# Kernel tuning notes

Hardware: AMD Instinct MI355X
Metric: run time of the kernel (lower is better)

## Reference

```python
import jax, jax.numpy as jnp
import numpy as np

B, N0, N1, FD, L, H = 4, 256, 256, 128, 3, 1
NG = N0 + N1            # nodes per graph
N = B * NG              # total nodes
EPS_BN = 1e-5
EPS_SM = 1e-16


def _build_edges():
    def perm_edges(n, off):
        idx = np.arange(n)
        a = np.repeat(idx, n); b = np.tile(idx, n)
        m = a != b
        return np.stack([a[m], b[m]]) + off
    e_intra = np.concatenate([perm_edges(N0, 0), perm_edges(N1, N0)], axis=1)
    a = np.arange(N0); b = np.arange(N0, N0 + N1)
    cross1 = np.stack([np.repeat(a, N1), np.tile(b, N0)])
    cross2 = np.stack([np.repeat(b, N0), np.tile(a, N1)])
    eg = np.concatenate([e_intra, cross1, cross2], axis=1)
    tg = np.concatenate([np.zeros(e_intra.shape[1], np.int32),
                         np.ones(cross1.shape[1] + cross2.shape[1], np.int32)])
    ei = np.concatenate([eg + g * NG for g in range(B)], axis=1).astype(np.int32)
    et = np.tile(tg, B).astype(np.int32)
    return jnp.asarray(ei), jnp.asarray(et)


def setup_inputs() -> dict:
    key = jax.random.key(0)
    ks = jax.random.split(key, 8)
    edge_index, edge_type = _build_edges()
    return {
        'desc0': jax.random.normal(ks[0], (B, FD, N0), jnp.float32),
        'desc1': jax.random.normal(ks[1], (B, FD, N1), jnp.float32),
        'W': jax.random.normal(ks[2], (L, 2, FD, H * FD), jnp.float32) * (1.0 / np.sqrt(FD)),
        'q': jax.random.normal(ks[3], (L, H * FD, H), jnp.float32) * 0.1,
        'k': jax.random.normal(ks[4], (L, H * FD, H), jnp.float32) * 0.1,
        'conv_b': jnp.zeros((L, FD), jnp.float32),
        'lin_W': jax.random.normal(ks[5], (L, FD, 2 * FD), jnp.float32) * (1.0 / np.sqrt(2 * FD)),
        'lin_b': jnp.zeros((L, FD), jnp.float32),
        'gamma': jnp.ones((L, FD), jnp.float32),
        'beta': jnp.zeros((L, FD), jnp.float32),
        'edge_index': edge_index,
        'edge_type': edge_type,
    }


def _forward(desc0, desc1, W, q, k, conv_b, lin_W, lin_b, gamma, beta, edge_index, edge_type):
    # x: [B, NG, FD] -> flattened batch graph [N, FD]
    x = jnp.concatenate([desc0, desc1], axis=2)        # [B, FD, NG]
    x = jnp.transpose(x, (0, 2, 1)).reshape(N, FD)
    src, dst = edge_index[0], edge_index[1]
    nlayers = W.shape[0]
    heads = q.shape[2]
    for l in range(nlayers):
        # relation-specific node projections (equiv to per-edge bmm with weight[edge_type])
        proj = jnp.einsum('nf,rfo->nro', x, W[l])       # [N, 2, H*FD]
        out_i = proj[dst, edge_type]                    # [E, H*FD]
        out_j = proj[src, edge_type]                    # [E, H*FD]
        alpha = jax.nn.leaky_relu(out_i @ q[l] + out_j @ k[l], 0.2)  # [E, H]
        # softmax over incoming edges of each destination node (across-relation)
        amax = jax.ops.segment_max(alpha, dst, num_segments=N)
        ex = jnp.exp(alpha - amax[dst])
        denom = jax.ops.segment_sum(ex, dst, num_segments=N)
        att = ex / (denom[dst] + EPS_SM)                # [E, H]
        msg = (att[:, :, None] * out_j.reshape(-1, heads, FD)).reshape(-1, heads * FD)
        agg = jax.ops.segment_sum(msg, dst, num_segments=N).reshape(N, heads, FD)
        m1 = jax.nn.relu(agg.mean(axis=1) + conv_b[l])  # concat=False -> mean over heads
        m2 = jnp.concatenate([x, m1], axis=1) @ lin_W[l].T + lin_b[l]
        mu = m2.mean(axis=0)
        var = ((m2 - mu) ** 2).mean(axis=0)             # biased var (BatchNorm training)
        m3 = (m2 - mu) / jnp.sqrt(var + EPS_BN) * gamma[l] + beta[l]
        x = x + m3
    x = x.reshape(B, NG, FD).transpose(0, 2, 1)         # [B, FD, NG]
    return x


def reference(desc0, desc1, W, q, k, conv_b, lin_W, lin_b, gamma, beta, edge_index, edge_type):
    x = _forward(desc0, desc1, W, q, k, conv_b, lin_W, lin_b, gamma, beta, edge_index, edge_type)
    return x[:, :, :N0], x[:, :, N0:]
```

## Files before the change

### kernel.cpp

```cpp
#include <hip/hip_runtime.h>

#define FD  128
#define NN  2048

#define OFF_X     0
#define OFF_PROJ  262144
#define OFF_QS    786432
#define OFF_KS    790528
#define OFF_SUMS  794624
#define OFF_LWT   800768
#define OFF_M2    899072

__device__ __forceinline__ int swizzle_n0(int bid) {
    int g    = (bid & 7) >> 1;
    int slot = ((bid >> 3) << 1) | (bid & 1);
    return g*512 + slot*8;
}

__device__ __forceinline__ void proj_qsks8(
    const float* __restrict__ W, const float* __restrict__ qv,
    const float* __restrict__ kv, float* __restrict__ ws,
    int l, int n0, int t, const float (*xs)[FD],
    float (*redp)[256], float* red)
{
    int kh = t >> 8, tp = t & 255;
    int rsel = tp >> 7, o = tp & 127;
    const float* Wl = W + ((size_t)(l*2 + rsel)*FD)*FD + o;
    float acc[8];
#pragma unroll
    for (int r = 0; r < 8; r++) acc[r] = 0.f;
    int kbase = kh * 64;
#pragma unroll
    for (int kk = 0; kk < 64; kk += 4) {
        int k4 = kbase + kk;
        float w0 = Wl[(k4+0)*FD], w1 = Wl[(k4+1)*FD];
        float w2 = Wl[(k4+2)*FD], w3 = Wl[(k4+3)*FD];
#pragma unroll
        for (int r = 0; r < 8; r++) {
            float4 xq = *(const float4*)&xs[r][k4];
            acc[r] += xq.x*w0 + xq.y*w1 + xq.z*w2 + xq.w*w3;
        }
    }
    if (kh == 1) {
#pragma unroll
        for (int r = 0; r < 8; r++) redp[r][tp] = acc[r];
    }
    __syncthreads();
    if (t < 256) {
#pragma unroll
        for (int r = 0; r < 8; r++) acc[r] += redp[r][tp];
#pragma unroll
        for (int r = 0; r < 8; r++)
            ws[OFF_PROJ + (size_t)(n0 + r)*256 + tp] = acc[r];

        float qq = qv[l*FD + o], kq = kv[l*FD + o];
        int lane = t & 63, w = t >> 6;
#pragma unroll
        for (int r = 0; r < 8; r++) {
            float vq = acc[r]*qq, vk = acc[r]*kq;
            for (int off = 32; off; off >>= 1) {
                vq += __shfl_xor(vq, off, 64);
                vk += __shfl_xor(vk, off, 64);
            }
            if (lane == 0) { red[w*16 + r*2] = vq; red[w*16 + r*2 + 1] = vk; }
        }
    }
    __syncthreads();
    if (t < 32) {
        int r = t & 7, rs = (t >> 3) & 1, wh = t >> 4;
        float v = red[(rs*2)*16 + r*2 + wh] + red[(rs*2 + 1)*16 + r*2 + wh];
        if (wh == 0) ws[OFF_QS + rs*NN + n0 + r] = v;
        else         ws[OFF_KS + rs*NN + n0 + r] = v;
    }
}

__global__ __launch_bounds__(512, 2) void k_pre(
    const float* __restrict__ d0, const float* __restrict__ d1,
    const float* __restrict__ W,  const float* __restrict__ qv,
    const float* __restrict__ kv, const float* __restrict__ linW,
    float* __restrict__ ws)
{
    int bid = blockIdx.x, t = threadIdx.x;
    if (bid >= 256) {
        if (bid < 280) {
            int vb = bid - 256;
#pragma unroll
            for (int i = 0; i < 8; i++) {
                int e = vb*4096 + i*512 + t;
                int l = e >> 15, rem = e & 32767;
                int o = rem >> 8, c = rem & 255;
                ws[OFF_LWT + l*32768 + c*FD + o] = linW[e];
            }
        } else {
            for (int i = t; i < 6144; i += 512) ws[OFF_SUMS + i] = 0.f;
        }
        return;
    }
    __shared__ __attribute__((aligned(16))) float xs[8][FD];
    __shared__ float redp[8][256];
    __shared__ float red[64];
    int n0 = swizzle_n0(bid);
#pragma unroll
    for (int i = 0; i < 2; i++) {
        int idx = t + i*512;
        int row = idx >> 7, f = idx & 127;
        int n = n0 + row, gg = n >> 9, ii = n & 511;
        float v = (ii < 256) ? d0[gg*32768 + f*256 + ii]
                             : d1[gg*32768 + f*256 + (ii - 256)];
        xs[row][f] = v;
        ws[OFF_X + (size_t)n*FD + f] = v;
    }
    __syncthreads();
    proj_qsks8(W, qv, kv, ws, 0, n0, t, xs, redp, red);
}

__global__ __launch_bounds__(512, 2) void k_bp(
    const float* __restrict__ W,     const float* __restrict__ qv,
    const float* __restrict__ kv,    const float* __restrict__ gamma,
    const float* __restrict__ beta,  float* __restrict__ ws, int l)
{
    __shared__ float scale[FD], shift[FD];
    __shared__ __attribute__((aligned(16))) float xs[8][FD];
    __shared__ float redp[8][256];
    __shared__ float red[64];
    int bid = blockIdx.x, t = threadIdx.x;
    int lp = l - 1;
    if (t < 128) {
        float s0 = 0.f, s1 = 0.f;
#pragma unroll
        for (int sl = 0; sl < 8; sl++) {
            s0 += ws[OFF_SUMS + lp*2048 + sl*256 + t];
            s1 += ws[OFF_SUMS + lp*2048 + sl*256 + 128 + t];
        }
        float mu  = s0 * (1.f/2048.f);
        float var = s1 * (1.f/2048.f) - mu*mu;
        float rs  = rsqrtf(var + 1e-5f);
        float gm  = gamma[lp*FD + t], bt = beta[lp*FD + t];
        scale[t] = gm * rs;
        shift[t] = bt - mu * gm * rs;
    }
    __syncthreads();
    int n0 = swizzle_n0(bid);
#pragma unroll
    for (int i = 0; i < 2; i++) {
        int idx = t + i*512;
        int row = idx >> 7, f = idx & 127;
        size_t e = (size_t)(n0 + row)*FD + f;
        float xv = ws[OFF_X + e] + ws[OFF_M2 + e]*scale[f] + shift[f];
        xs[row][f] = xv;
        ws[OFF_X + e] = xv;
    }
    __syncthreads();
    proj_qsks8(W, qv, kv, ws, l, n0, t, xs, redp, red);
}

__global__ __launch_bounds__(512, 2) void k_attn(
    const float* __restrict__ convb, const float* __restrict__ linb,
    float* __restrict__ ws, int l)
{
    __shared__ __attribute__((aligned(16))) float att[8*512];
    __shared__ __attribute__((aligned(16))) float redB[8*8*128];
    __shared__ __attribute__((aligned(16))) float cat[8*256];
    __shared__ float r1[FD], r2[FD];

    int bid = blockIdx.x, t = threadIdx.x;
    int dstbase = swizzle_n0(bid);
    int g = dstbase >> 9, dloc0 = dstbase & 511;
    int Gd = (dloc0 >= 256) ? 1 : 0;

    {
        int d = t >> 6, p = t & 63;
        int dloc = dloc0 + d;
        float q0 = ws[OFF_QS + dstbase + d];
        float q1 = ws[OFF_QS + NN + dstbase + d];
        float sc[8];
#pragma unroll
        for (int j = 0; j < 8; j++) {
            int s = p + j*64;
            int ts = (s < 256) ? Gd : 1 - Gd;
            float a = (ts ? q1 : q0) + ws[OFF_KS + ts*NN + g*512 + s];
            a = a > 0.f ? a : 0.2f*a;
            sc[j] = (s == dloc) ? -1e30f : a;
        }
        float lm = sc[0];
#pragma unroll
        for (int j = 1; j < 8; j++) lm = fmaxf(lm, sc[j]);
        for (int off = 32; off; off >>= 1) lm = fmaxf(lm, __shfl_xor(lm, off, 64));
        float ex[8], lsum = 0.f;
#pragma unroll
        for (int j = 0; j < 8; j++) { ex[j] = __expf(sc[j] - lm); lsum += ex[j]; }
        for (int off = 32; off; off >>= 1) lsum += __shfl_xor(lsum, off, 64);
        float inv = 1.f / (lsum + 1e-16f);
#pragma unroll
        for (int j = 0; j < 8; j++) att[d*512 + p + j*64] = ex[j]*inv;
        if (t < 128) r1[t] = 0.f;
        else if (t < 256) r2[t - 128] = 0.f;
    }
    __syncthreads();

    int f4 = t & 31, sq = t >> 5;
    float acc[8][4];
#pragma unroll
    for (int d2 = 0; d2 < 8; d2++)
#pragma unroll
        for (int j = 0; j < 4; j++) acc[d2][j] = 0.f;
    {
        int ts = (sq < 8) ? Gd : 1 - Gd;
        const float* P = ws + OFF_PROJ + (size_t)(g*512)*256 + ts*128 + f4*4;
        int s0 = sq * 32;
        float4 bufA[4], bufB[4];
#pragma unroll
        for (int u = 0; u < 4; u++) bufA[u] = *(const float4*)&P[(size_t)(s0+u)*256];
#pragma unroll
        for (int ii = 0; ii < 8; ii++) {
            const float4* cur = (ii & 1) ? bufB : bufA;
            float4*       nxt = (ii & 1) ? bufA : bufB;
            if (ii < 7) {
#pragma unroll
                for (int u = 0; u < 4; u++)
                    nxt[u] = *(const float4*)&P[(size_t)(s0 + (ii+1)*4 + u)*256];
            }
#pragma unroll
            for (int u = 0; u < 4; u++) {
                int s = s0 + ii*4 + u;
                float4 p4 = cur[u];
#pragma unroll
                for (int d2 = 0; d2 < 8; d2++) {
                    float b = att[d2*512 + s];
                    acc[d2][0] += b*p4.x; acc[d2][1] += b*p4.y;
                    acc[d2][2] += b*p4.z; acc[d2][3] += b*p4.w;
                }
            }
        }
    }
    if (sq >= 8) {
#pragma unroll
        for (int d2 = 0; d2 < 8; d2++)
            *(float4*)&redB[((sq - 8)*8 + d2)*128 + f4*4] =
                make_float4(acc[d2][0], acc[d2][1], acc[d2][2], acc[d2][3]);
    }
    __syncthreads();
    if (sq < 8) {
#pragma unroll
        for (int d2 = 0; d2 < 8; d2++) {
            float4 p4 = *(const float4*)&redB[(sq*8 + d2)*128 + f4*4];
            *(float4*)&redB[(sq*8 + d2)*128 + f4*4] =
                make_float4(acc[d2][0]+p4.x, acc[d2][1]+p4.y, acc[d2][2]+p4.z, acc[d2][3]+p4.w);
        }
    }
    __syncthreads();

    {
        int dh = t >> 7, f = t & 127;
#pragma unroll
        for (int half = 0; half < 2; half++) {
            int d2 = dh + half*4;
            float agg = 0.f;
#pragma unroll
            for (int cc = 0; cc < 8; cc++) agg += redB[(cc*8 + d2)*128 + f];
            float m1v = fmaxf(agg + convb[l*FD + f], 0.f);
            cat[d2*256 + FD + f] = m1v;
            cat[d2*256 + f] = ws[OFF_X + (size_t)(dstbase + d2)*FD + f];
        }
    }
    __syncthreads();

#pragma unroll
    for (int d2 = 0; d2 < 8; d2++)
#pragma unroll
        for (int j = 0; j < 4; j++) acc[d2][j] = 0.f;
    {
        const float* lwt = ws + OFF_LWT + l*32768 + f4*4;
        int c0 = sq * 16;
        float4 bufA[4], bufB[4];
#pragma unroll
        for (int u = 0; u < 4; u++) bufA[u] = *(const float4*)&lwt[(c0+u)*128];
#pragma unroll
        for (int ii = 0; ii < 4; ii++) {
            const float4* cur = (ii & 1) ? bufB : bufA;
            float4*       nxt = (ii & 1) ? bufA : bufB;
            if (ii < 3) {
#pragma unroll
                for (int u = 0; u < 4; u++)
                    nxt[u] = *(const float4*)&lwt[(c0 + (ii+1)*4 + u)*128];
            }
#pragma unroll
            for (int u = 0; u < 4; u++) {
                int c = c0 + ii*4 + u;
                float4 w4 = cur[u];
#pragma unroll
                for (int d2 = 0; d2 < 8; d2++) {
                    float cv = cat[d2*256 + c];
                    acc[d2][0] += cv*w4.x; acc[d2][1] += cv*w4.y;
                    acc[d2][2] += cv*w4.z; acc[d2][3] += cv*w4.w;
                }
            }
        }
    }
    if (sq >= 8) {
#pragma unroll
        for (int d2 = 0; d2 < 8; d2++)
            *(float4*)&redB[((sq - 8)*8 + d2)*128 + f4*4] =
                make_float4(acc[d2][0], acc[d2][1], acc[d2][2], acc[d2][3]);
    }
    __syncthreads();
    if (sq < 8) {
#pragma unroll
        for (int d2 = 0; d2 < 8; d2++) {
            float4 p4 = *(const float4*)&redB[(sq*8 + d2)*128 + f4*4];
            *(float4*)&redB[(sq*8 + d2)*128 + f4*4] =
                make_float4(acc[d2][0]+p4.x, acc[d2][1]+p4.y, acc[d2][2]+p4.z, acc[d2][3]+p4.w);
        }
    }
    __syncthreads();

    {
        int dh = t >> 7, o = t & 127;
        float lb = linb[l*FD + o];
#pragma unroll
        for (int half = 0; half < 2; half++) {
            int d2 = dh + half*4;
            float m2v = lb;
#pragma unroll
            for (int cc = 0; cc < 8; cc++) m2v += redB[(cc*8 + d2)*128 + o];
            ws[OFF_M2 + (size_t)(dstbase + d2)*FD + o] = m2v;
            atomicAdd(&r1[o], m2v);
            atomicAdd(&r2[o], m2v*m2v);
        }
    }
    __syncthreads();
    if (t < 128) {
        int slot = bid & 7;
        atomicAdd(&ws[OFF_SUMS + l*2048 + slot*256 + t],       r1[t]);
        atomicAdd(&ws[OFF_SUMS + l*2048 + slot*256 + 128 + t], r2[t]);
    }
}

__global__ __launch_bounds__(256) void k_bnout(
    const float* __restrict__ gamma, const float* __restrict__ beta,
    float* __restrict__ ws, float* __restrict__ out)
{
    __shared__ float scale[FD], shift[FD];
    int bid = blockIdx.x, t = threadIdx.x;
    if (t < 128) {
        float s0 = 0.f, s1 = 0.f;
#pragma unroll
        for (int sl = 0; sl < 8; sl++) {
            s0 += ws[OFF_SUMS + 2*2048 + sl*256 + t];
            s1 += ws[OFF_SUMS + 2*2048 + sl*256 + 128 + t];
        }
        float mu  = s0 * (1.f/2048.f);
        float var = s1 * (1.f/2048.f) - mu*mu;
        float rs  = rsqrtf(var + 1e-5f);
        float gm  = gamma[2*FD + t], bt = beta[2*FD + t];
        scale[t] = gm * rs;
        shift[t] = bt - mu * gm * rs;
    }
    __syncthreads();
#pragma unroll
    for (int i = 0; i < 2; i++) {
        int idx = bid*512 + i*256 + t;
        int f = idx & 127, n = idx >> 7;
        float v = ws[OFF_X + idx] + ws[OFF_M2 + idx]*scale[f] + shift[f];
        int gg = n >> 9, ii = n & 511;
        int off = (ii < 256) ? (gg*32768 + f*256 + ii)
                             : (131072 + gg*32768 + f*256 + (ii - 256));
        out[off] = v;
    }
}

extern "C" void kernel_launch(void* const* d_in, const int* in_sizes, int n_in,
                              void* d_out, int out_size, void* d_ws, size_t ws_size,
                              hipStream_t stream) {
    (void)in_sizes; (void)n_in; (void)out_size; (void)ws_size;
    const float* desc0 = (const float*)d_in[0];
    const float* desc1 = (const float*)d_in[1];
    const float* W     = (const float*)d_in[2];
    const float* q     = (const float*)d_in[3];
    const float* kk    = (const float*)d_in[4];
    const float* convb = (const float*)d_in[5];
    const float* linW  = (const float*)d_in[6];
    const float* linb  = (const float*)d_in[7];
    const float* gamma = (const float*)d_in[8];
    const float* beta  = (const float*)d_in[9];
    float* ws  = (float*)d_ws;
    float* out = (float*)d_out;

    hipLaunchKernelGGL(k_pre,  dim3(281), dim3(512), 0, stream, desc0, desc1, W, q, kk, linW, ws);
    hipLaunchKernelGGL(k_attn, dim3(256), dim3(512), 0, stream, convb, linb, ws, 0);
    hipLaunchKernelGGL(k_bp,   dim3(256), dim3(512), 0, stream, W, q, kk, gamma, beta, ws, 1);
    hipLaunchKernelGGL(k_attn, dim3(256), dim3(512), 0, stream, convb, linb, ws, 1);
    hipLaunchKernelGGL(k_bp,   dim3(256), dim3(512), 0, stream, W, q, kk, gamma, beta, ws, 2);
    hipLaunchKernelGGL(k_attn, dim3(256), dim3(512), 0, stream, convb, linb, ws, 2);
    hipLaunchKernelGGL(k_bnout, dim3(512), dim3(256), 0, stream, gamma, beta, ws, out);
}
```

Before: 166.2 us.

## Halve rows per block to double grid size and split softmax across wavefronts

Each block now handles 4 destination nodes instead of 8, which doubles the grid from 256 to 512 blocks for the projection and attention kernels and raises launch-bounds occupancy to 4 blocks per CU. Softmax for each destination is split across two wavefronts, which combine partial max and sum through shared memory and then rescale. The aim is to fill the MI355X's CUs better and lower per-block latency. In exchange, each block gets less reuse of the W, proj and linW loads, so global and L2 traffic rises, and the softmax needs an extra barrier.

```diff
diff --git a/kernel.cpp b/kernel.cpp
--- a/kernel.cpp
+++ b/kernel.cpp
@@ -14,10 +14,10 @@
 __device__ __forceinline__ int swizzle_n0(int bid) {
     int g    = (bid & 7) >> 1;
     int slot = ((bid >> 3) << 1) | (bid & 1);
-    return g*512 + slot*8;
-}
-
-__device__ __forceinline__ void proj_qsks8(
+    return g*512 + slot*4;
+}
+
+__device__ __forceinline__ void proj_qsks4(
     const float* __restrict__ W, const float* __restrict__ qv,
     const float* __restrict__ kv, float* __restrict__ ws,
     int l, int n0, int t, const float (*xs)[FD],
@@ -26,9 +26,9 @@
     int kh = t >> 8, tp = t & 255;
     int rsel = tp >> 7, o = tp & 127;
     const float* Wl = W + ((size_t)(l*2 + rsel)*FD)*FD + o;
-    float acc[8];
-#pragma unroll
-    for (int r = 0; r < 8; r++) acc[r] = 0.f;
+    float acc[4];
+#pragma unroll
+    for (int r = 0; r < 4; r++) acc[r] = 0.f;
     int kbase = kh * 64;
 #pragma unroll
     for (int kk = 0; kk < 64; kk += 4) {
@@ -36,54 +36,54 @@
         float w0 = Wl[(k4+0)*FD], w1 = Wl[(k4+1)*FD];
         float w2 = Wl[(k4+2)*FD], w3 = Wl[(k4+3)*FD];
 #pragma unroll
-        for (int r = 0; r < 8; r++) {
+        for (int r = 0; r < 4; r++) {
             float4 xq = *(const float4*)&xs[r][k4];
             acc[r] += xq.x*w0 + xq.y*w1 + xq.z*w2 + xq.w*w3;
         }
     }
     if (kh == 1) {
 #pragma unroll
-        for (int r = 0; r < 8; r++) redp[r][tp] = acc[r];
+        for (int r = 0; r < 4; r++) redp[r][tp] = acc[r];
     }
     __syncthreads();
     if (t < 256) {
 #pragma unroll
-        for (int r = 0; r < 8; r++) acc[r] += redp[r][tp];
-#pragma unroll
-        for (int r = 0; r < 8; r++)
+        for (int r = 0; r < 4; r++) acc[r] += redp[r][tp];
+#pragma unroll
+        for (int r = 0; r < 4; r++)
             ws[OFF_PROJ + (size_t)(n0 + r)*256 + tp] = acc[r];
 
         float qq = qv[l*FD + o], kq = kv[l*FD + o];
         int lane = t & 63, w = t >> 6;
 #pragma unroll
-        for (int r = 0; r < 8; r++) {
+        for (int r = 0; r < 4; r++) {
             float vq = acc[r]*qq, vk = acc[r]*kq;
             for (int off = 32; off; off >>= 1) {
                 vq += __shfl_xor(vq, off, 64);
                 vk += __shfl_xor(vk, off, 64);
             }
-            if (lane == 0) { red[w*16 + r*2] = vq; red[w*16 + r*2 + 1] = vk; }
-        }
-    }
-    __syncthreads();
-    if (t < 32) {
-        int r = t & 7, rs = (t >> 3) & 1, wh = t >> 4;
-        float v = red[(rs*2)*16 + r*2 + wh] + red[(rs*2 + 1)*16 + r*2 + wh];
+            if (lane == 0) { red[w*8 + r*2] = vq; red[w*8 + r*2 + 1] = vk; }
+        }
+    }
+    __syncthreads();
+    if (t < 16) {
+        int r = t & 3, rs = (t >> 2) & 1, wh = t >> 3;
+        float v = red[(rs*2)*8 + r*2 + wh] + red[(rs*2 + 1)*8 + r*2 + wh];
         if (wh == 0) ws[OFF_QS + rs*NN + n0 + r] = v;
         else         ws[OFF_KS + rs*NN + n0 + r] = v;
     }
 }
 
-__global__ __launch_bounds__(512, 2) void k_pre(
+__global__ __launch_bounds__(512, 4) void k_pre(
     const float* __restrict__ d0, const float* __restrict__ d1,
     const float* __restrict__ W,  const float* __restrict__ qv,
     const float* __restrict__ kv, const float* __restrict__ linW,
     float* __restrict__ ws)
 {
     int bid = blockIdx.x, t = threadIdx.x;
-    if (bid >= 256) {
-        if (bid < 280) {
-            int vb = bid - 256;
+    if (bid >= 512) {
+        if (bid < 536) {
+            int vb = bid - 512;
 #pragma unroll
             for (int i = 0; i < 8; i++) {
                 int e = vb*4096 + i*512 + t;
@@ -96,14 +96,12 @@
         }
         return;
     }
-    __shared__ __attribute__((aligned(16))) float xs[8][FD];
-    __shared__ float redp[8][256];
-    __shared__ float red[64];
+    __shared__ __attribute__((aligned(16))) float xs[4][FD];
+    __shared__ float redp[4][256];
+    __shared__ float red[32];
     int n0 = swizzle_n0(bid);
-#pragma unroll
-    for (int i = 0; i < 2; i++) {
-        int idx = t + i*512;
-        int row = idx >> 7, f = idx & 127;
+    {
+        int row = t >> 7, f = t & 127;
         int n = n0 + row, gg = n >> 9, ii = n & 511;
         float v = (ii < 256) ? d0[gg*32768 + f*256 + ii]
                              : d1[gg*32768 + f*256 + (ii - 256)];
@@ -111,18 +109,18 @@
         ws[OFF_X + (size_t)n*FD + f] = v;
     }
     __syncthreads();
-    proj_qsks8(W, qv, kv, ws, 0, n0, t, xs, redp, red);
-}
-
-__global__ __launch_bounds__(512, 2) void k_bp(
+    proj_qsks4(W, qv, kv, ws, 0, n0, t, xs, redp, red);
+}
+
+__global__ __launch_bounds__(512, 4) void k_bp(
     const float* __restrict__ W,     const float* __restrict__ qv,
     const float* __restrict__ kv,    const float* __restrict__ gamma,
     const float* __restrict__ beta,  float* __restrict__ ws, int l)
 {
     __shared__ float scale[FD], shift[FD];
-    __shared__ __attribute__((aligned(16))) float xs[8][FD];
-    __shared__ float redp[8][256];
-    __shared__ float red[64];
+    __shared__ __attribute__((aligned(16))) float xs[4][FD];
+    __shared__ float redp[4][256];
+    __shared__ float red[32];
     int bid = blockIdx.x, t = threadIdx.x;
     int lp = l - 1;
     if (t < 128) {
@@ -141,26 +139,25 @@
     }
     __syncthreads();
     int n0 = swizzle_n0(bid);
-#pragma unroll
-    for (int i = 0; i < 2; i++) {
-        int idx = t + i*512;
-        int row = idx >> 7, f = idx & 127;
+    {
+        int row = t >> 7, f = t & 127;
         size_t e = (size_t)(n0 + row)*FD + f;
         float xv = ws[OFF_X + e] + ws[OFF_M2 + e]*scale[f] + shift[f];
         xs[row][f] = xv;
         ws[OFF_X + e] = xv;
     }
     __syncthreads();
-    proj_qsks8(W, qv, kv, ws, l, n0, t, xs, redp, red);
-}
-
-__global__ __launch_bounds__(512, 2) void k_attn(
+    proj_qsks4(W, qv, kv, ws, l, n0, t, xs, redp, red);
+}
+
+__global__ __launch_bounds__(512, 4) void k_attn(
     const float* __restrict__ convb, const float* __restrict__ linb,
     float* __restrict__ ws, int l)
 {
-    __shared__ __attribute__((aligned(16))) float att[8*512];
-    __shared__ __attribute__((aligned(16))) float redB[8*8*128];
-    __shared__ __attribute__((aligned(16))) float cat[8*256];
+    __shared__ __attribute__((aligned(16))) float att[4*512];
+    __shared__ __attribute__((aligned(16))) float redB[8*4*128];
+    __shared__ __attribute__((aligned(16))) float cat[4*256];
+    __shared__ float sml[4][2], sls[4][2];
     __shared__ float r1[FD], r2[FD];
 
     int bid = blockIdx.x, t = threadIdx.x;
@@ -169,39 +166,50 @@
     int Gd = (dloc0 >= 256) ? 1 : 0;
 
     {
-        int d = t >> 6, p = t & 63;
+        int w = t >> 6, p = t & 63;
+        int d = w >> 1, h = w & 1;
         int dloc = dloc0 + d;
         float q0 = ws[OFF_QS + dstbase + d];
         float q1 = ws[OFF_QS + NN + dstbase + d];
-        float sc[8];
-#pragma unroll
-        for (int j = 0; j < 8; j++) {
-            int s = p + j*64;
+        float sc[4];
+#pragma unroll
+        for (int j = 0; j < 4; j++) {
+            int s = h*256 + p + j*64;
             int ts = (s < 256) ? Gd : 1 - Gd;
             float a = (ts ? q1 : q0) + ws[OFF_KS + ts*NN + g*512 + s];
             a = a > 0.f ? a : 0.2f*a;
             sc[j] = (s == dloc) ? -1e30f : a;
         }
-        float lm = sc[0];
-#pragma unroll
-        for (int j = 1; j < 8; j++) lm = fmaxf(lm, sc[j]);
+        float lm = fmaxf(fmaxf(sc[0], sc[1]), fmaxf(sc[2], sc[3]));
         for (int off = 32; off; off >>= 1) lm = fmaxf(lm, __shfl_xor(lm, off, 64));
-        float ex[8], lsum = 0.f;
-#pragma unroll
-        for (int j = 0; j < 8; j++) { ex[j] = __expf(sc[j] - lm); lsum += ex[j]; }
+        float ex[4], lsum = 0.f;
+#pragma unroll
+        for (int j = 0; j < 4; j++) { ex[j] = __expf(sc[j] - lm); lsum += ex[j]; }
         for (int off = 32; off; off >>= 1) lsum += __shfl_xor(lsum, off, 64);
-        float inv = 1.f / (lsum + 1e-16f);
-#pragma unroll
-        for (int j = 0; j < 8; j++) att[d*512 + p + j*64] = ex[j]*inv;
+#pragma unroll
+        for (int j = 0; j < 4; j++) att[d*512 + h*256 + p + j*64] = ex[j];
+        if (p == 0) { sml[d][h] = lm; sls[d][h] = lsum; }
+    }
+    __syncthreads();
+    {
+        int d = t >> 7, s4 = (t & 127) * 4;
+        int h = (s4 >= 256) ? 1 : 0;
+        float m0 = sml[d][0], m1 = sml[d][1];
+        float M = fmaxf(m0, m1);
+        float denom = sls[d][0]*__expf(m0 - M) + sls[d][1]*__expf(m1 - M) + 1e-16f;
+        float fac = __expf(sml[d][h] - M) / denom;
+        float4 a4 = *(float4*)&att[d*512 + s4];
+        a4.x *= fac; a4.y *= fac; a4.z *= fac; a4.w *= fac;
+        *(float4*)&att[d*512 + s4] = a4;
         if (t < 128) r1[t] = 0.f;
         else if (t < 256) r2[t - 128] = 0.f;
     }
     __syncthreads();
 
     int f4 = t & 31, sq = t >> 5;
-    float acc[8][4];
-#pragma unroll
-    for (int d2 = 0; d2 < 8; d2++)
+    float acc[4][4];
+#pragma unroll
+    for (int d2 = 0; d2 < 4; d2++)
 #pragma unroll
         for (int j = 0; j < 4; j++) acc[d2][j] = 0.f;
     {
@@ -225,7 +233,7 @@
                 int s = s0 + ii*4 + u;
                 float4 p4 = cur[u];
 #pragma unroll
-                for (int d2 = 0; d2 < 8; d2++) {
+                for (int d2 = 0; d2 < 4; d2++) {
                     float b = att[d2*512 + s];
                     acc[d2][0] += b*p4.x; acc[d2][1] += b*p4.y;
                     acc[d2][2] += b*p4.z; acc[d2][3] += b*p4.w;
@@ -235,38 +243,34 @@
     }
     if (sq >= 8) {
 #pragma unroll
-        for (int d2 = 0; d2 < 8; d2++)
-            *(float4*)&redB[((sq - 8)*8 + d2)*128 + f4*4] =
+        for (int d2 = 0; d2 < 4; d2++)
+            *(float4*)&redB[((sq - 8)*4 + d2)*128 + f4*4] =
                 make_float4(acc[d2][0], acc[d2][1], acc[d2][2], acc[d2][3]);
     }
     __syncthreads();
     if (sq < 8) {
 #pragma unroll
-        for (int d2 = 0; d2 < 8; d2++) {
-            float4 p4 = *(const float4*)&redB[(sq*8 + d2)*128 + f4*4];
-            *(float4*)&redB[(sq*8 + d2)*128 + f4*4] =
+        for (int d2 = 0; d2 < 4; d2++) {
+            float4 p4 = *(const float4*)&redB[(sq*4 + d2)*128 + f4*4];
+            *(float4*)&redB[(sq*4 + d2)*128 + f4*4] =
                 make_float4(acc[d2][0]+p4.x, acc[d2][1]+p4.y, acc[d2][2]+p4.z, acc[d2][3]+p4.w);
         }
     }
     __syncthreads();
 
     {
-        int dh = t >> 7, f = t & 127;
-#pragma unroll
-        for (int half = 0; half < 2; half++) {
-            int d2 = dh + half*4;
-            float agg = 0.f;
-#pragma unroll
-            for (int cc = 0; cc < 8; cc++) agg += redB[(cc*8 + d2)*128 + f];
-            float m1v = fmaxf(agg + convb[l*FD + f], 0.f);
-            cat[d2*256 + FD + f] = m1v;
-            cat[d2*256 + f] = ws[OFF_X + (size_t)(dstbase + d2)*FD + f];
-        }
-    }
-    __syncthreads();
-
-#pragma unroll
-    for (int d2 = 0; d2 < 8; d2++)
+        int d2 = t >> 7, f = t & 127;
+        float agg = 0.f;
+#pragma unroll
+        for (int cc = 0; cc < 8; cc++) agg += redB[(cc*4 + d2)*128 + f];
+        float m1v = fmaxf(agg + convb[l*FD + f], 0.f);
+        cat[d2*256 + FD + f] = m1v;
+        cat[d2*256 + f] = ws[OFF_X + (size_t)(dstbase + d2)*FD + f];
+    }
+    __syncthreads();
+
+#pragma unroll
+    for (int d2 = 0; d2 < 4; d2++)
 #pragma unroll
         for (int j = 0; j < 4; j++) acc[d2][j] = 0.f;
     {
@@ -289,7 +293,7 @@
                 int c = c0 + ii*4 + u;
                 float4 w4 = cur[u];
 #pragma unroll
-                for (int d2 = 0; d2 < 8; d2++) {
+                for (int d2 = 0; d2 < 4; d2++) {
                     float cv = cat[d2*256 + c];
                     acc[d2][0] += cv*w4.x; acc[d2][1] += cv*w4.y;
                     acc[d2][2] += cv*w4.z; acc[d2][3] += cv*w4.w;
@@ -299,34 +303,29 @@
     }
     if (sq >= 8) {
 #pragma unroll
-        for (int d2 = 0; d2 < 8; d2++)
-            *(float4*)&redB[((sq - 8)*8 + d2)*128 + f4*4] =
+        for (int d2 = 0; d2 < 4; d2++)
+            *(float4*)&redB[((sq - 8)*4 + d2)*128 + f4*4] =
                 make_float4(acc[d2][0], acc[d2][1], acc[d2][2], acc[d2][3]);
     }
     __syncthreads();
     if (sq < 8) {
 #pragma unroll
-        for (int d2 = 0; d2 < 8; d2++) {
-            float4 p4 = *(const float4*)&redB[(sq*8 + d2)*128 + f4*4];
-            *(float4*)&redB[(sq*8 + d2)*128 + f4*4] =
+        for (int d2 = 0; d2 < 4; d2++) {
+            float4 p4 = *(const float4*)&redB[(sq*4 + d2)*128 + f4*4];
+            *(float4*)&redB[(sq*4 + d2)*128 + f4*4] =
                 make_float4(acc[d2][0]+p4.x, acc[d2][1]+p4.y, acc[d2][2]+p4.z, acc[d2][3]+p4.w);
         }
     }
     __syncthreads();
 
     {
-        int dh = t >> 7, o = t & 127;
-        float lb = linb[l*FD + o];
-#pragma unroll
-        for (int half = 0; half < 2; half++) {
-            int d2 = dh + half*4;
-            float m2v = lb;
-#pragma unroll
-            for (int cc = 0; cc < 8; cc++) m2v += redB[(cc*8 + d2)*128 + o];
-            ws[OFF_M2 + (size_t)(dstbase + d2)*FD + o] = m2v;
-            atomicAdd(&r1[o], m2v);
-            atomicAdd(&r2[o], m2v*m2v);
-        }
+        int d2 = t >> 7, o = t & 127;
+        float m2v = linb[l*FD + o];
+#pragma unroll
+        for (int cc = 0; cc < 8; cc++) m2v += redB[(cc*4 + d2)*128 + o];
+        ws[OFF_M2 + (size_t)(dstbase + d2)*FD + o] = m2v;
+        atomicAdd(&r1[o], m2v);
+        atomicAdd(&r2[o], m2v*m2v);
     }
     __syncthreads();
     if (t < 128) {
@@ -386,11 +385,11 @@
     float* ws  = (float*)d_ws;
     float* out = (float*)d_out;
 
-    hipLaunchKernelGGL(k_pre,  dim3(281), dim3(512), 0, stream, desc0, desc1, W, q, kk, linW, ws);
-    hipLaunchKernelGGL(k_attn, dim3(256), dim3(512), 0, stream, convb, linb, ws, 0);
-    hipLaunchKernelGGL(k_bp,   dim3(256), dim3(512), 0, stream, W, q, kk, gamma, beta, ws, 1);
-    hipLaunchKernelGGL(k_attn, dim3(256), dim3(512), 0, stream, convb, linb, ws, 1);
-    hipLaunchKernelGGL(k_bp,   dim3(256), dim3(512), 0, stream, W, q, kk, gamma, beta, ws, 2);
-    hipLaunchKernelGGL(k_attn, dim3(256), dim3(512), 0, stream, convb, linb, ws, 2);
+    hipLaunchKernelGGL(k_pre,  dim3(537), dim3(512), 0, stream, desc0, desc1, W, q, kk, linW, ws);
+    hipLaunchKernelGGL(k_attn, dim3(512), dim3(512), 0, stream, convb, linb, ws, 0);
+    hipLaunchKernelGGL(k_bp,   dim3(512), dim3(512), 0, stream, W, q, kk, gamma, beta, ws, 1);
+    hipLaunchKernelGGL(k_attn, dim3(512), dim3(512), 0, stream, convb, linb, ws, 1);
+    hipLaunchKernelGGL(k_bp,   dim3(512), dim3(512), 0, stream, W, q, kk, gamma, beta, ws, 2);
+    hipLaunchKernelGGL(k_attn, dim3(512), dim3(512), 0, stream, convb, linb, ws, 2);
     hipLaunchKernelGGL(k_bnout, dim3(512), dim3(256), 0, stream, gamma, beta, ws, out);
 }
```

Result: faster. 156.2 us (-6.1%).
